# Optimization experiments

Hardware: AMD Instinct MI355X
Metric: run time of the kernel (lower is better)

## Reference

```python
import jax, jax.numpy as jnp
import numpy as np

B, V, VD = 4, 256, 3
H_DIM, N_HEADS = 512, 8
HEAD_DIM = H_DIM // N_HEADS
LN_EPS = 1e-5


def _ln(x, g, b):
    m = jnp.mean(x, axis=-1, keepdims=True)
    v = jnp.var(x, axis=-1, keepdims=True)
    return (x - m) * jax.lax.rsqrt(v + LN_EPS) * g + b


def setup_inputs() -> dict:
    key = jax.random.key(0)
    ks = jax.random.split(key, 20)
    s = lambda fan_in: 1.0 / np.sqrt(fan_in)
    return {
        "vertices": jax.random.normal(ks[0], (B, V, VD), jnp.float32),
        # vertex_proj: Linear(3 -> 512)
        "wp": jax.random.uniform(ks[1], (H_DIM, VD), jnp.float32, -s(VD), s(VD)),
        "bp": jax.random.uniform(ks[2], (H_DIM,), jnp.float32, -s(VD), s(VD)),
        # MultiheadAttention packed in-proj (3E, E) and out-proj (E, E)
        "in_w": jax.random.uniform(ks[3], (3 * H_DIM, H_DIM), jnp.float32, -s(H_DIM), s(H_DIM)),
        "in_b": jnp.zeros((3 * H_DIM,), jnp.float32),
        "out_w": jax.random.uniform(ks[4], (H_DIM, H_DIM), jnp.float32, -s(H_DIM), s(H_DIM)),
        "out_b": jnp.zeros((H_DIM,), jnp.float32),
        # edge_mlp: Linear(1024->512), LN(512), GELU, Linear(512->256), LN(256), GELU, Linear(256->1)
        "w1": jax.random.uniform(ks[5], (H_DIM, 2 * H_DIM), jnp.float32, -s(2 * H_DIM), s(2 * H_DIM)),
        "b1": jax.random.uniform(ks[6], (H_DIM,), jnp.float32, -s(2 * H_DIM), s(2 * H_DIM)),
        "g1": jnp.ones((H_DIM,), jnp.float32),
        "be1": jnp.zeros((H_DIM,), jnp.float32),
        "w2": jax.random.uniform(ks[7], (H_DIM // 2, H_DIM), jnp.float32, -s(H_DIM), s(H_DIM)),
        "b2": jax.random.uniform(ks[8], (H_DIM // 2,), jnp.float32, -s(H_DIM), s(H_DIM)),
        "g2": jnp.ones((H_DIM // 2,), jnp.float32),
        "be2": jnp.zeros((H_DIM // 2,), jnp.float32),
        "w3": jax.random.uniform(ks[9], (1, H_DIM // 2), jnp.float32, -s(H_DIM // 2), s(H_DIM // 2)),
        "b3": jax.random.uniform(ks[10], (1,), jnp.float32, -s(H_DIM // 2), s(H_DIM // 2)),
    }


def reference(vertices, wp, bp, in_w, in_b, out_w, out_b,
              w1, b1, g1, be1, w2, b2, g2, be2, w3, b3):
    # vertex projection: [B, V, H]
    x = jnp.einsum("bvd,hd->bvh", vertices, wp) + bp

    # self-attention (eval mode: dropout off)
    qkv = jnp.einsum("bvh,eh->bve", x, in_w) + in_b  # [B, V, 3H]
    q, k, v = jnp.split(qkv, 3, axis=-1)
    q = q.reshape(B, V, N_HEADS, HEAD_DIM)
    k = k.reshape(B, V, N_HEADS, HEAD_DIM)
    v = v.reshape(B, V, N_HEADS, HEAD_DIM)
    scores = jnp.einsum("bqnd,bknd->bnqk", q, k) / np.sqrt(HEAD_DIM)
    attn = jax.nn.softmax(scores, axis=-1)
    ctx = jnp.einsum("bnqk,bknd->bqnd", attn, v).reshape(B, V, H_DIM)
    attended = jnp.einsum("bvh,oh->bvo", ctx, out_w) + out_b
    x = x + attended  # residual

    # gather all upper-triangular vertex pairs: E = V*(V-1)/2
    ii, jj = jnp.triu_indices(V, k=1)
    v1 = x[:, ii, :]  # [B, E, H]
    v2 = x[:, jj, :]
    e = jnp.concatenate([v1, v2], axis=-1)  # [B, E, 2H]

    # edge MLP (exact-erf GELU like torch default)
    h = jnp.einsum("beh,oh->beo", e, w1) + b1
    h = jax.nn.gelu(_ln(h, g1, be1), approximate=False)
    h = jnp.einsum("beh,oh->beo", h, w2) + b2
    h = jax.nn.gelu(_ln(h, g2, be2), approximate=False)
    logits = jnp.einsum("beh,oh->beo", h, w3) + b3  # [B, E, 1]
    return jax.nn.sigmoid(logits[..., 0])  # [B, E]
```

## Files before the change

### kernel.cpp

```cpp
#include <hip/hip_runtime.h>
#include <hip/hip_bf16.h>
#include <hip/hip_fp16.h>

#define B_  4
#define V_  256
#define H_  512
#define E_  32640

typedef _Float16 half8 __attribute__((ext_vector_type(8)));
typedef float    f32x4 __attribute__((ext_vector_type(4)));

__device__ __forceinline__ float gelu_f(float x) {
    float u = x * 0.70710678118654752f;
    float a = fabsf(u);
    float t = __builtin_amdgcn_rcpf(fmaf(0.3275911f, a, 1.0f));
    float poly = t * fmaf(t, fmaf(t, fmaf(t, fmaf(t, 1.061405429f, -1.453152027f),
                                          1.421413741f), -0.284496736f), 0.254829592f);
    float ex = __expf(-u * u);
    float erfa = fmaf(-poly, ex, 1.0f);
    float erfu = copysignf(erfa, u);
    return 0.5f * x * (1.0f + erfu);
}

__device__ __forceinline__ float wred_add(float v) {
    #pragma unroll
    for (int off = 32; off > 0; off >>= 1) v += __shfl_xor(v, off, 64);
    return v;
}

__device__ __forceinline__ void split16(float v, _Float16* hi, _Float16* lo) {
    _Float16 h = (_Float16)v;
    *hi = h; *lo = (_Float16)(v - (float)h);
}

__device__ __forceinline__ size_t fmoff(int R, int row, int k) {
    return ((size_t)(k >> 3) * R + row) * 8 + (k & 7);
}

__global__ void k_setup(const float* __restrict__ verts, const float* __restrict__ wp,
                        const float* __restrict__ bp, float* __restrict__ x,
                        _Float16* __restrict__ xfh, _Float16* __restrict__ xfl,
                        const float* __restrict__ w2, _Float16* __restrict__ w2f,
                        int2* __restrict__ etab,
                        const float* __restrict__ in_w, _Float16* __restrict__ iwfh, _Float16* __restrict__ iwfl,
                        const float* __restrict__ out_w, _Float16* __restrict__ owfh, _Float16* __restrict__ owfl,
                        const float* __restrict__ w1, _Float16* __restrict__ w1fh, _Float16* __restrict__ w1fl) {
    int t = blockIdx.x * 256 + threadIdx.x;
    if (t < 524288) {
        int row = t >> 9, k = t & 511;
        const float* vr = verts + row * 3;
        const float* wr = wp + k * 3;
        float val = vr[0] * wr[0] + vr[1] * wr[1] + vr[2] * wr[2] + bp[k];
        x[t] = val;
        size_t fo = fmoff(1024, row, k);
        split16(val, xfh + fo, xfl + fo);
        return;
    }
    t -= 524288;
    if (t < 131072) {
        int col = t >> 9, k = t & 511;
        w2f[fmoff(256, col, k)] = (_Float16)w2[t];
        return;
    }
    t -= 131072;
    if (t < 32640) {
        double disc = (double)(2 * V_ - 1) * (2 * V_ - 1) - 8.0 * (double)t;
        int i = (int)((2 * V_ - 1 - sqrt(disc)) * 0.5);
        if (i < 0) i = 0;
        if (i > V_ - 2) i = V_ - 2;
        while (i < V_ - 2 && (i + 1) * (2 * V_ - 1 - (i + 1)) / 2 <= t) ++i;
        while (i > 0 && i * (2 * V_ - 1 - i) / 2 > t) --i;
        int j = t - i * (2 * V_ - 1 - i) / 2 + i + 1;
        etab[t] = make_int2(i, j);
        return;
    }
    t -= 32640;
    if (t < 786432) {
        int col = t >> 9, k = t & 511;
        size_t fo = fmoff(1536, col, k);
        split16(in_w[t], iwfh + fo, iwfl + fo);
        return;
    }
    t -= 786432;
    if (t < 262144) {
        int col = t >> 9, k = t & 511;
        size_t fo = fmoff(512, col, k);
        split16(out_w[t], owfh + fo, owfl + fo);
        return;
    }
    t -= 262144;
    if (t < 524288) {
        int col = t >> 9, k = t & 511;
        float v = (col < 512) ? w1[col * 1024 + k] : w1[(col - 512) * 1024 + 512 + k];
        size_t fo = fmoff(1024, col, k);
        split16(v, w1fh + fo, w1fl + fo);
    }
}

template<int MODE>
__global__ __launch_bounds__(256) void k_gemm_sp(
        const _Float16* __restrict__ Ahf, const _Float16* __restrict__ Alf,
        const _Float16* __restrict__ Whf, const _Float16* __restrict__ Wlf,
        const float* __restrict__ bias, const float* __restrict__ res,
        float* __restrict__ C, _Float16* __restrict__ Fh, _Float16* __restrict__ Fl,
        float* __restrict__ C2, _Float16* __restrict__ F2h, int N)
{
    const int tid = threadIdx.x;
    const int w = tid >> 6, l = tid & 63;
    const int lr = l & 15, lg = l >> 4;
    const int mg = w >> 1, ng = w & 1;
    const int row0 = blockIdx.y * 64 + mg * 32;
    const int col0 = blockIdx.x * 64 + ng * 32;

    f32x4 acc[2][2] = {};
    for (int kk = 0; kk < 16; ++kk) {
        const int kg = kk * 4 + lg;
        half8 ah[2], al[2], bh[2], bl[2];
        #pragma unroll
        for (int mi = 0; mi < 2; ++mi) {
            size_t off = ((size_t)kg * 1024 + row0 + mi * 16 + lr) * 8;
            ah[mi] = *(const half8*)(Ahf + off);
            al[mi] = *(const half8*)(Alf + off);
        }
        #pragma unroll
        for (int ni = 0; ni < 2; ++ni) {
            size_t off = ((size_t)kg * N + col0 + ni * 16 + lr) * 8;
            bh[ni] = *(const half8*)(Whf + off);
            bl[ni] = *(const half8*)(Wlf + off);
        }
        #pragma unroll
        for (int mi = 0; mi < 2; ++mi)
            #pragma unroll
            for (int ni = 0; ni < 2; ++ni) {
                acc[mi][ni] = __builtin_amdgcn_mfma_f32_16x16x32_f16(ah[mi], bh[ni], acc[mi][ni], 0, 0, 0);
                acc[mi][ni] = __builtin_amdgcn_mfma_f32_16x16x32_f16(ah[mi], bl[ni], acc[mi][ni], 0, 0, 0);
                acc[mi][ni] = __builtin_amdgcn_mfma_f32_16x16x32_f16(al[mi], bh[ni], acc[mi][ni], 0, 0, 0);
            }
    }
    #pragma unroll
    for (int mi = 0; mi < 2; ++mi)
        #pragma unroll
        for (int ni = 0; ni < 2; ++ni)
            #pragma unroll
            for (int r = 0; r < 4; ++r) {
                int row = row0 + mi * 16 + lg * 4 + r;
                int col = col0 + ni * 16 + lr;
                float v = acc[mi][ni][r];
                if (MODE == 1) {
                    size_t idx = (size_t)row * 512 + col;
                    v += bias[col] + res[idx];
                    C[idx] = v;
                    size_t fo = fmoff(1024, row, col);
                    split16(v, Fh + fo, Fl + fo);
                } else if (MODE == 2) {
                    if (col < 512) {
                        size_t idx = (size_t)row * 512 + col;
                        v += bias[col];
                        C[idx] = v;
                        Fh[fmoff(1024, row, col)] = (_Float16)v;
                    } else {
                        int c2 = col - 512;
                        C2[(size_t)row * 512 + c2] = v;
                        F2h[fmoff(1024, row, c2)] = (_Float16)v;
                    }
                } else {
                    v += bias[col];
                    int bb = row >> 8, tok = row & 255;
                    _Float16 hi = (_Float16)v;
                    _Float16 lo = (_Float16)(v - (float)hi);
                    if (col < 1024) {
                        int hp = col >> 6, d = col & 63;
                        size_t off = (((size_t)(bb * 16 + hp) * 8 + (d >> 3)) * 256 + tok) * 8 + (d & 7);
                        Fh[off] = hi; Fl[off] = lo;
                    } else {
                        int c = col - 1024, hp = c >> 6, d = c & 63;
                        size_t off = (((size_t)(bb * 8 + hp) * 32 + (tok >> 3)) * 64 + d) * 8 + (tok & 7);
                        ((_Float16*)C2)[off] = hi; F2h[off] = lo;
                    }
                }
            }
}

__global__ __launch_bounds__(256) void k_attn(
        const _Float16* __restrict__ QKh, const _Float16* __restrict__ QKl,
        const _Float16* __restrict__ Vh, const _Float16* __restrict__ Vl,
        _Float16* __restrict__ cfh, _Float16* __restrict__ cfl)
{
    extern __shared__ unsigned char smem[];
    const int tid = threadIdx.x;
    const int w = tid >> 6, l = tid & 63;
    const int lr = l & 15, lg = l >> 4;
    const int bh = blockIdx.x >> 2;
    const int b = bh >> 3, h = bh & 7;
    const int qb = blockIdx.x & 3;
    const int q0 = qb * 64 + w * 16;
    unsigned char* ph_base = smem + w * 16384;
    unsigned char* pl_base = ph_base + 8192;

    const size_t qbase = (size_t)(b * 16 + h) * 8;
    const size_t kbase = (size_t)(b * 16 + 8 + h) * 8;
    const size_t vbase = (size_t)(b * 8 + h) * 32;

    half8 qh[2], ql[2];
    #pragma unroll
    for (int ks = 0; ks < 2; ++ks) {
        size_t off = ((qbase + ks * 4 + lg) * 256 + q0 + lr) * 8;
        qh[ks] = *(const half8*)(QKh + off);
        ql[ks] = *(const half8*)(QKl + off);
    }

    f32x4 sc[16];
    #pragma unroll
    for (int kt = 0; kt < 16; ++kt) {
        f32x4 a = {};
        #pragma unroll
        for (int ks = 0; ks < 2; ++ks) {
            size_t off = ((kbase + ks * 4 + lg) * 256 + kt * 16 + lr) * 8;
            half8 kh = *(const half8*)(QKh + off);
            half8 kl = *(const half8*)(QKl + off);
            a = __builtin_amdgcn_mfma_f32_16x16x32_f16(qh[ks], kh, a, 0, 0, 0);
            a = __builtin_amdgcn_mfma_f32_16x16x32_f16(qh[ks], kl, a, 0, 0, 0);
            a = __builtin_amdgcn_mfma_f32_16x16x32_f16(ql[ks], kh, a, 0, 0, 0);
        }
        sc[kt] = a;
    }

    float mr[4] = {-1e30f, -1e30f, -1e30f, -1e30f};
    #pragma unroll
    for (int kt = 0; kt < 16; ++kt)
        #pragma unroll
        for (int r = 0; r < 4; ++r) mr[r] = fmaxf(mr[r], sc[kt][r]);
    #pragma unroll
    for (int off = 1; off < 16; off <<= 1)
        #pragma unroll
        for (int r = 0; r < 4; ++r) mr[r] = fmaxf(mr[r], __shfl_xor(mr[r], off, 64));

    float Ls[4] = {};
    #pragma unroll
    for (int kt = 0; kt < 16; ++kt)
        #pragma unroll
        for (int r = 0; r < 4; ++r) {
            float p = __expf((sc[kt][r] - mr[r]) * 0.125f);
            Ls[r] += p;
            _Float16 hp = (_Float16)p;
            _Float16 lp = (_Float16)(p - (float)hp);
            const int row = lg * 4 + r;
            unsigned off = row * 512 + (((unsigned)(kt * 16 + lr) * 2) ^ ((row & 7) << 4));
            *(_Float16*)(ph_base + off) = hp;
            *(_Float16*)(pl_base + off) = lp;
        }
    #pragma unroll
    for (int off = 1; off < 16; off <<= 1)
        #pragma unroll
        for (int r = 0; r < 4; ++r) Ls[r] += __shfl_xor(Ls[r], off, 64);

    __syncthreads();

    f32x4 o[4] = {};
    #pragma unroll
    for (int ks = 0; ks < 8; ++ks) {
        unsigned roff = lr * 512 + (((unsigned)(ks * 64 + lg * 16)) ^ ((lr & 7) << 4));
        half8 pah = *(const half8*)(ph_base + roff);
        half8 pal = *(const half8*)(pl_base + roff);
        #pragma unroll
        for (int nt = 0; nt < 4; ++nt) {
            size_t off = ((vbase + ks * 4 + lg) * 64 + nt * 16 + lr) * 8;
            half8 vbh = *(const half8*)(Vh + off);
            half8 vbl = *(const half8*)(Vl + off);
            o[nt] = __builtin_amdgcn_mfma_f32_16x16x32_f16(pah, vbh, o[nt], 0, 0, 0);
            o[nt] = __builtin_amdgcn_mfma_f32_16x16x32_f16(pah, vbl, o[nt], 0, 0, 0);
            o[nt] = __builtin_amdgcn_mfma_f32_16x16x32_f16(pal, vbh, o[nt], 0, 0, 0);
        }
    }

    float Linv[4];
    #pragma unroll
    for (int r = 0; r < 4; ++r) Linv[r] = 1.0f / Ls[r];
    #pragma unroll
    for (int nt = 0; nt < 4; ++nt)
        #pragma unroll
        for (int r = 0; r < 4; ++r) {
            float val = o[nt][r] * Linv[r];
            int row = b * 256 + q0 + lg * 4 + r;
            int col = h * 64 + nt * 16 + lr;
            size_t fo = fmoff(1024, row, col);
            split16(val, cfh + fo, cfl + fo);
        }
}

__global__ __launch_bounds__(256) void k_pair_stats(
        const _Float16* __restrict__ Ahf, const _Float16* __restrict__ Bhf,
        const float* __restrict__ Amat, const float* __restrict__ Bmat,
        float* __restrict__ P, float2* __restrict__ statsA, float2* __restrict__ statsB) {
    const int bid = blockIdx.x;
    const int tid = threadIdx.x;
    if (bid < 256) {
        const int t = bid * 4 + (tid >> 6);
        const int b = t >> 8, tt = t & 255;
        const int i0 = (tt >> 4) * 16, j0 = (tt & 15) * 16;
        const int l = tid & 63, lr = l & 15, lg = l >> 4;
        f32x4 acc = {};
        for (int kk = 0; kk < 16; ++kk) {
            const int kg = kk * 4 + lg;
            half8 af = *(const half8*)(Ahf + ((size_t)kg * 1024 + b * 256 + i0 + lr) * 8);
            half8 bf = *(const half8*)(Bhf + ((size_t)kg * 1024 + b * 256 + j0 + lr) * 8);
            acc = __builtin_amdgcn_mfma_f32_16x16x32_f16(af, bf, acc, 0, 0, 0);
        }
        #pragma unroll
        for (int r = 0; r < 4; ++r)
            P[((size_t)b << 16) + (size_t)(i0 + lg * 4 + r) * 256 + j0 + lr] = acc[r];
    } else {
        const int sid = bid - 256;
        const int slice = tid >> 4, lane = tid & 15;
        const int m = sid * 16 + slice;
        const float* src = (m < 1024 ? Amat + (size_t)m * 512 : Bmat + (size_t)(m - 1024) * 512);
        float s = 0.0f, sq = 0.0f;
        #pragma unroll
        for (int i = 0; i < 8; ++i) {
            f32x4 v = *(const f32x4*)(src + i * 64 + lane * 4);
            s  += v[0] + v[1] + v[2] + v[3];
            sq += v[0]*v[0] + v[1]*v[1] + v[2]*v[2] + v[3]*v[3];
        }
        #pragma unroll
        for (int off = 8; off > 0; off >>= 1) {
            s  += __shfl_xor(s, off, 64);
            sq += __shfl_xor(sq, off, 64);
        }
        if (lane == 0) {
            if (m < 1024) statsA[m] = make_float2(s, sq);
            else          statsB[m - 1024] = make_float2(s, sq);
        }
    }
}

__global__ __launch_bounds__(512, 4) void k_edge(
        const float* __restrict__ Am, const float* __restrict__ Bm,
        const _Float16* __restrict__ w2f,
        const float* __restrict__ g1, const float* __restrict__ be1,
        const float* __restrict__ b2, const float* __restrict__ g2,
        const float* __restrict__ be2, const float* __restrict__ w3,
        const float* __restrict__ b3, const int2* __restrict__ etab,
        const float2* __restrict__ statsA, const float2* __restrict__ statsB,
        const float* __restrict__ P, float* __restrict__ out)
{
    extern __shared__ unsigned char smem[];
    const int tid = threadIdx.x;
    const int w = tid >> 6;
    const int l = tid & 63;
    const int bid0 = blockIdx.x;
    const int swz = (bid0 & 7) * 255 + (bid0 >> 3);
    const int b  = swz / 510;
    const int eb = swz % 510;

    {
        const int el = l >> 3;
        const int kq = l & 7;
        const int e  = w * 8 + el;
        int2 ij = etab[eb * 64 + e];
        float2 sa = statsA[b * 256 + ij.x];
        float2 sb = statsB[b * 256 + ij.y];
        float pij = P[((size_t)b << 16) + ((size_t)ij.x << 8) + ij.y];
        float mean = (sa.x + sb.x) * (1.0f / 512.0f);
        float ex2  = (sa.y + sb.y + 2.0f * pij) * (1.0f / 512.0f);
        float rstd = rsqrtf(ex2 - mean * mean + 1e-5f);
        const float* ar = Am + (((size_t)(b * 256 + ij.x)) << 9);
        const float* br = Bm + (((size_t)(b * 256 + ij.y)) << 9);
        #pragma unroll
        for (int t = 0; t < 8; ++t) {
            const int kg = kq + 8 * t;
            const int k0 = kg * 8;
            f32x4 a0 = *(const f32x4*)(ar + k0);
            f32x4 a1 = *(const f32x4*)(ar + k0 + 4);
            f32x4 c0 = *(const f32x4*)(br + k0);
            f32x4 c1 = *(const f32x4*)(br + k0 + 4);
            f32x4 ga = *(const f32x4*)(g1 + k0);
            f32x4 gb = *(const f32x4*)(g1 + k0 + 4);
            f32x4 ea = *(const f32x4*)(be1 + k0);
            f32x4 ebv= *(const f32x4*)(be1 + k0 + 4);
            half8 hv;
            #pragma unroll
            for (int c = 0; c < 4; ++c) {
                float xa = ((a0[c] + c0[c]) - mean) * rstd * ga[c] + ea[c];
                float xb = ((a1[c] + c1[c]) - mean) * rstd * gb[c] + ebv[c];
                hv[c]     = (_Float16)gelu_f(xa);
                hv[c + 4] = (_Float16)gelu_f(xb);
            }
            *(half8*)(smem + kg * 1024 + ((e ^ (kg & 7)) << 4)) = hv;
        }
    }
    __syncthreads();

    f32x4 acc[4][2] = {};
    const int lg = l >> 4, lr = l & 15;
    const int col0 = w * 32;
    #pragma unroll
    for (int kk = 0; kk < 16; ++kk) {
        const int kg = kk * 4 + lg;
        half8 bf[2];
        #pragma unroll
        for (int ni = 0; ni < 2; ++ni)
            bf[ni] = *(const half8*)(w2f + ((size_t)kg * 256 + col0 + ni * 16 + lr) * 8);
        half8 af[4];
        #pragma unroll
        for (int mi = 0; mi < 4; ++mi)
            af[mi] = *(const half8*)(smem + kg * 1024 + (((mi * 16 + lr) ^ (kg & 7)) << 4));
        #pragma unroll
        for (int mi = 0; mi < 4; ++mi)
            #pragma unroll
            for (int ni = 0; ni < 2; ++ni)
                acc[mi][ni] = __builtin_amdgcn_mfma_f32_16x16x32_f16(af[mi], bf[ni], acc[mi][ni], 0, 0, 0);
    }
    __syncthreads();

    #pragma unroll
    for (int ni = 0; ni < 2; ++ni) {
        const int col = col0 + ni * 16 + lr;
        const float bb = b2[col];
        #pragma unroll
        for (int mi = 0; mi < 4; ++mi)
            #pragma unroll
            for (int r = 0; r < 4; ++r) {
                const int e = mi * 16 + lg * 4 + r;
                *(float*)(smem + e * 1024 + col * 4) = acc[mi][ni][r] + bb;
            }
    }
    __syncthreads();

    {
        const int o0 = l * 4;
        f32x4 g2v = *(const f32x4*)(g2 + o0);
        f32x4 e2v = *(const f32x4*)(be2 + o0);
        f32x4 w3v = *(const f32x4*)(w3 + o0);
        float b3s = b3[0];
        #pragma unroll
        for (int el = 0; el < 8; ++el) {
            const int e = w * 8 + el;
            f32x4 h = *(const f32x4*)(smem + e * 1024 + o0 * 4);
            float s  = h[0] + h[1] + h[2] + h[3];
            float sq = h[0]*h[0] + h[1]*h[1] + h[2]*h[2] + h[3]*h[3];
            s = wred_add(s); sq = wred_add(sq);
            float mean = s * (1.0f / 256.0f);
            float rstd = rsqrtf(sq * (1.0f / 256.0f) - mean * mean + 1e-5f);
            float part = 0.0f;
            #pragma unroll
            for (int c = 0; c < 4; ++c) {
                float xx = (h[c] - mean) * rstd * g2v[c] + e2v[c];
                part += gelu_f(xx) * w3v[c];
            }
            part = wred_add(part);
            if (l == 0)
                out[(size_t)b * E_ + eb * 64 + e] = 1.0f / (1.0f + __expf(-(part + b3s)));
        }
    }
}

extern "C" void kernel_launch(void* const* d_in, const int* in_sizes, int n_in,
                              void* d_out, int out_size, void* d_ws, size_t ws_size,
                              hipStream_t stream) {
    const float* verts = (const float*)d_in[0];
    const float* wp    = (const float*)d_in[1];
    const float* bp    = (const float*)d_in[2];
    const float* in_w  = (const float*)d_in[3];
    const float* in_b  = (const float*)d_in[4];
    const float* out_w = (const float*)d_in[5];
    const float* out_b = (const float*)d_in[6];
    const float* w1    = (const float*)d_in[7];
    const float* b1    = (const float*)d_in[8];
    const float* g1    = (const float*)d_in[9];
    const float* be1   = (const float*)d_in[10];
    const float* w2    = (const float*)d_in[11];
    const float* b2    = (const float*)d_in[12];
    const float* g2    = (const float*)d_in[13];
    const float* be2   = (const float*)d_in[14];
    const float* w3    = (const float*)d_in[15];
    const float* b3    = (const float*)d_in[16];
    float* out = (float*)d_out;

    const size_t MB = 1 << 20;
    char* W = (char*)d_ws;
    float*    x     = (float*)(W + 0);
    _Float16* xfh   = (_Float16*)(W + 2*MB);
    _Float16* xfl   = (_Float16*)(W + 3*MB);
    _Float16* QKfh  = (_Float16*)(W + 4*MB);
    _Float16* QKfl  = (_Float16*)(W + 6*MB);
    _Float16* Vfh   = (_Float16*)(W + 8*MB);
    _Float16* Vfl   = (_Float16*)(W + 9*MB);
    float*    Amat  = (float*)(W + 4*MB);
    float*    Bmat  = (float*)(W + 6*MB);
    _Float16* Ahf   = (_Float16*)(W + 8*MB);
    _Float16* Bhf   = (_Float16*)(W + 9*MB);
    _Float16* ctxfh = (_Float16*)(W + 10*MB);
    _Float16* ctxfl = (_Float16*)(W + 11*MB);
    _Float16* w2f   = (_Float16*)(W + 12*MB);
    int2*     etab  = (int2*)(W + 12*MB + 256*1024);
    float2*   statsA= (float2*)(W + 12*MB + 512*1024);
    float2*   statsB= (float2*)(W + 12*MB + 520*1024);
    _Float16* iwfh  = (_Float16*)(W + 13*MB);
    _Float16* iwfl  = (_Float16*)(W + 13*MB + 1536*1024);
    _Float16* owfh  = (_Float16*)(W + 16*MB);
    _Float16* owfl  = (_Float16*)(W + 16*MB + 512*1024);
    _Float16* w1fh  = (_Float16*)(W + 17*MB);
    _Float16* w1fl  = (_Float16*)(W + 18*MB);
    float*    P     = (float*)(W + 19*MB);

    k_setup<<<dim3(8832), dim3(256), 0, stream>>>(verts, wp, bp, x, xfh, xfl,
                                                  w2, w2f, etab, in_w, iwfh, iwfl,
                                                  out_w, owfh, owfl, w1, w1fh, w1fl);
    k_gemm_sp<3><<<dim3(24, 16), dim3(256), 0, stream>>>(xfh, xfl, iwfh, iwfl, in_b, nullptr,
                                                         nullptr, QKfh, QKfl, (float*)Vfh, Vfl, 1536);
    k_attn<<<dim3(128), dim3(256), 65536, stream>>>(QKfh, QKfl, Vfh, Vfl, ctxfh, ctxfl);
    k_gemm_sp<1><<<dim3(8, 16), dim3(256), 0, stream>>>(ctxfh, ctxfl, owfh, owfl, out_b, x,
                                                        x, xfh, xfl, nullptr, nullptr, 512);
    k_gemm_sp<2><<<dim3(16, 16), dim3(256), 0, stream>>>(xfh, xfl, w1fh, w1fl, b1, nullptr,
                                                         Amat, Ahf, nullptr, Bmat, Bhf, 1024);
    k_pair_stats<<<dim3(384), dim3(256), 0, stream>>>(Ahf, Bhf, Amat, Bmat, P, statsA, statsB);
    k_edge<<<dim3(B_ * 510), dim3(512), 65536, stream>>>(Amat, Bmat, w2f,
                                                         g1, be1, b2, g2, be2, w3, b3,
                                                         etab, statsA, statsB, P, out);
}
```

Measured before the change: 265.7 us.

## Halve edge-kernel tile and interleave fp16 hi/lo pairs for attention buffers

The edge MLP kernel now handles 32 edges per block instead of 64. That halves its shared memory to 32KB, doubles the grid, and raises the launch-bounds occupancy hint from 4 to 8. The goal is more resident blocks to hide latency, at the cost of reading the w2 weights twice as often overall. Separately, the QKV, V and context split-fp16 buffers now store hi and lo interleaved as one 32-bit word. This replaces paired 16-bit stores and separate loads with single packed accesses plus some bit unpacking in the attention and out-projection GEMM.

```diff
diff --git a/kernel.cpp b/kernel.cpp
--- a/kernel.cpp
+++ b/kernel.cpp
@@ -9,6 +9,7 @@
 
 typedef _Float16 half8 __attribute__((ext_vector_type(8)));
 typedef float    f32x4 __attribute__((ext_vector_type(4)));
+typedef unsigned int uint4v __attribute__((ext_vector_type(4)));
 
 __device__ __forceinline__ float gelu_f(float x) {
     float u = x * 0.70710678118654752f;
@@ -31,6 +32,26 @@
 __device__ __forceinline__ void split16(float v, _Float16* hi, _Float16* lo) {
     _Float16 h = (_Float16)v;
     *hi = h; *lo = (_Float16)(v - (float)h);
+}
+
+__device__ __forceinline__ unsigned packf(float v) {
+    _Float16 h = (_Float16)v;
+    _Float16 l = (_Float16)(v - (float)h);
+    unsigned hu = (unsigned)__builtin_bit_cast(unsigned short, h);
+    unsigned lu = (unsigned)__builtin_bit_cast(unsigned short, l);
+    return hu | (lu << 16);
+}
+
+__device__ __forceinline__ void unpk8(const unsigned* p, half8& hi, half8& lo) {
+    uint4v a = *(const uint4v*)p;
+    uint4v b = *(const uint4v*)(p + 4);
+    uint4v hw, lw;
+    hw[0] = (a[0] & 0xFFFFu) | (a[1] << 16);  lw[0] = (a[0] >> 16) | (a[1] & 0xFFFF0000u);
+    hw[1] = (a[2] & 0xFFFFu) | (a[3] << 16);  lw[1] = (a[2] >> 16) | (a[3] & 0xFFFF0000u);
+    hw[2] = (b[0] & 0xFFFFu) | (b[1] << 16);  lw[2] = (b[0] >> 16) | (b[1] & 0xFFFF0000u);
+    hw[3] = (b[2] & 0xFFFFu) | (b[3] << 16);  lw[3] = (b[2] >> 16) | (b[3] & 0xFFFF0000u);
+    hi = __builtin_bit_cast(half8, hw);
+    lo = __builtin_bit_cast(half8, lw);
 }
 
 __device__ __forceinline__ size_t fmoff(int R, int row, int k) {
@@ -119,8 +140,12 @@
         #pragma unroll
         for (int mi = 0; mi < 2; ++mi) {
             size_t off = ((size_t)kg * 1024 + row0 + mi * 16 + lr) * 8;
-            ah[mi] = *(const half8*)(Ahf + off);
-            al[mi] = *(const half8*)(Alf + off);
+            if (MODE == 1) {
+                unpk8((const unsigned*)Ahf + off, ah[mi], al[mi]);
+            } else {
+                ah[mi] = *(const half8*)(Ahf + off);
+                al[mi] = *(const half8*)(Alf + off);
+            }
         }
         #pragma unroll
         for (int ni = 0; ni < 2; ++ni) {
@@ -166,25 +191,22 @@
                 } else {
                     v += bias[col];
                     int bb = row >> 8, tok = row & 255;
-                    _Float16 hi = (_Float16)v;
-                    _Float16 lo = (_Float16)(v - (float)hi);
                     if (col < 1024) {
                         int hp = col >> 6, d = col & 63;
                         size_t off = (((size_t)(bb * 16 + hp) * 8 + (d >> 3)) * 256 + tok) * 8 + (d & 7);
-                        Fh[off] = hi; Fl[off] = lo;
+                        ((unsigned*)Fh)[off] = packf(v);
                     } else {
                         int c = col - 1024, hp = c >> 6, d = c & 63;
                         size_t off = (((size_t)(bb * 8 + hp) * 32 + (tok >> 3)) * 64 + d) * 8 + (tok & 7);
-                        ((_Float16*)C2)[off] = hi; F2h[off] = lo;
+                        ((unsigned*)C2)[off] = packf(v);
                     }
                 }
             }
 }
 
 __global__ __launch_bounds__(256) void k_attn(
-        const _Float16* __restrict__ QKh, const _Float16* __restrict__ QKl,
-        const _Float16* __restrict__ Vh, const _Float16* __restrict__ Vl,
-        _Float16* __restrict__ cfh, _Float16* __restrict__ cfl)
+        const unsigned* __restrict__ QKp, const unsigned* __restrict__ Vp,
+        unsigned* __restrict__ ctxp)
 {
     extern __shared__ unsigned char smem[];
     const int tid = threadIdx.x;
@@ -205,8 +227,7 @@
     #pragma unroll
     for (int ks = 0; ks < 2; ++ks) {
         size_t off = ((qbase + ks * 4 + lg) * 256 + q0 + lr) * 8;
-        qh[ks] = *(const half8*)(QKh + off);
-        ql[ks] = *(const half8*)(QKl + off);
+        unpk8(QKp + off, qh[ks], ql[ks]);
     }
 
     f32x4 sc[16];
@@ -216,8 +237,8 @@
         #pragma unroll
         for (int ks = 0; ks < 2; ++ks) {
             size_t off = ((kbase + ks * 4 + lg) * 256 + kt * 16 + lr) * 8;
-            half8 kh = *(const half8*)(QKh + off);
-            half8 kl = *(const half8*)(QKl + off);
+            half8 kh, kl;
+            unpk8(QKp + off, kh, kl);
             a = __builtin_amdgcn_mfma_f32_16x16x32_f16(qh[ks], kh, a, 0, 0, 0);
             a = __builtin_amdgcn_mfma_f32_16x16x32_f16(qh[ks], kl, a, 0, 0, 0);
             a = __builtin_amdgcn_mfma_f32_16x16x32_f16(ql[ks], kh, a, 0, 0, 0);
@@ -265,8 +286,8 @@
         #pragma unroll
         for (int nt = 0; nt < 4; ++nt) {
             size_t off = ((vbase + ks * 4 + lg) * 64 + nt * 16 + lr) * 8;
-            half8 vbh = *(const half8*)(Vh + off);
-            half8 vbl = *(const half8*)(Vl + off);
+            half8 vbh, vbl;
+            unpk8(Vp + off, vbh, vbl);
             o[nt] = __builtin_amdgcn_mfma_f32_16x16x32_f16(pah, vbh, o[nt], 0, 0, 0);
             o[nt] = __builtin_amdgcn_mfma_f32_16x16x32_f16(pah, vbl, o[nt], 0, 0, 0);
             o[nt] = __builtin_amdgcn_mfma_f32_16x16x32_f16(pal, vbh, o[nt], 0, 0, 0);
@@ -283,8 +304,7 @@
             float val = o[nt][r] * Linv[r];
             int row = b * 256 + q0 + lg * 4 + r;
             int col = h * 64 + nt * 16 + lr;
-            size_t fo = fmoff(1024, row, col);
-            split16(val, cfh + fo, cfl + fo);
+            ctxp[fmoff(1024, row, col)] = packf(val);
         }
 }
 
@@ -333,7 +353,7 @@
     }
 }
 
-__global__ __launch_bounds__(512, 4) void k_edge(
+__global__ __launch_bounds__(512, 8) void k_edge(
         const float* __restrict__ Am, const float* __restrict__ Bm,
         const _Float16* __restrict__ w2f,
         const float* __restrict__ g1, const float* __restrict__ be1,
@@ -348,15 +368,14 @@
     const int w = tid >> 6;
     const int l = tid & 63;
     const int bid0 = blockIdx.x;
-    const int swz = (bid0 & 7) * 255 + (bid0 >> 3);
-    const int b  = swz / 510;
-    const int eb = swz % 510;
+    const int swz = (bid0 & 7) * 510 + (bid0 >> 3);
+    const int b  = swz / 1020;
+    const int eb = swz % 1020;
 
     {
-        const int el = l >> 3;
-        const int kq = l & 7;
-        const int e  = w * 8 + el;
-        int2 ij = etab[eb * 64 + e];
+        const int e  = w * 4 + (l >> 4);
+        const int kq = l & 15;
+        int2 ij = etab[eb * 32 + e];
         float2 sa = statsA[b * 256 + ij.x];
         float2 sb = statsB[b * 256 + ij.y];
         float pij = P[((size_t)b << 16) + ((size_t)ij.x << 8) + ij.y];
@@ -366,8 +385,8 @@
         const float* ar = Am + (((size_t)(b * 256 + ij.x)) << 9);
         const float* br = Bm + (((size_t)(b * 256 + ij.y)) << 9);
         #pragma unroll
-        for (int t = 0; t < 8; ++t) {
-            const int kg = kq + 8 * t;
+        for (int t = 0; t < 4; ++t) {
+            const int kg = kq + 16 * t;
             const int k0 = kg * 8;
             f32x4 a0 = *(const f32x4*)(ar + k0);
             f32x4 a1 = *(const f32x4*)(ar + k0 + 4);
@@ -385,12 +404,12 @@
                 hv[c]     = (_Float16)gelu_f(xa);
                 hv[c + 4] = (_Float16)gelu_f(xb);
             }
-            *(half8*)(smem + kg * 1024 + ((e ^ (kg & 7)) << 4)) = hv;
+            *(half8*)(smem + kg * 512 + ((e ^ (kg & 7)) << 4)) = hv;
         }
     }
     __syncthreads();
 
-    f32x4 acc[4][2] = {};
+    f32x4 acc[2][2] = {};
     const int lg = l >> 4, lr = l & 15;
     const int col0 = w * 32;
     #pragma unroll
@@ -400,12 +419,12 @@
         #pragma unroll
         for (int ni = 0; ni < 2; ++ni)
             bf[ni] = *(const half8*)(w2f + ((size_t)kg * 256 + col0 + ni * 16 + lr) * 8);
-        half8 af[4];
-        #pragma unroll
-        for (int mi = 0; mi < 4; ++mi)
-            af[mi] = *(const half8*)(smem + kg * 1024 + (((mi * 16 + lr) ^ (kg & 7)) << 4));
-        #pragma unroll
-        for (int mi = 0; mi < 4; ++mi)
+        half8 af[2];
+        #pragma unroll
+        for (int mi = 0; mi < 2; ++mi)
+            af[mi] = *(const half8*)(smem + kg * 512 + (((mi * 16 + lr) ^ (kg & 7)) << 4));
+        #pragma unroll
+        for (int mi = 0; mi < 2; ++mi)
             #pragma unroll
             for (int ni = 0; ni < 2; ++ni)
                 acc[mi][ni] = __builtin_amdgcn_mfma_f32_16x16x32_f16(af[mi], bf[ni], acc[mi][ni], 0, 0, 0);
@@ -417,7 +436,7 @@
         const int col = col0 + ni * 16 + lr;
         const float bb = b2[col];
         #pragma unroll
-        for (int mi = 0; mi < 4; ++mi)
+        for (int mi = 0; mi < 2; ++mi)
             #pragma unroll
             for (int r = 0; r < 4; ++r) {
                 const int e = mi * 16 + lg * 4 + r;
@@ -433,8 +452,8 @@
         f32x4 w3v = *(const f32x4*)(w3 + o0);
         float b3s = b3[0];
         #pragma unroll
-        for (int el = 0; el < 8; ++el) {
-            const int e = w * 8 + el;
+        for (int el = 0; el < 4; ++el) {
+            const int e = w * 4 + el;
             f32x4 h = *(const f32x4*)(smem + e * 1024 + o0 * 4);
             float s  = h[0] + h[1] + h[2] + h[3];
             float sq = h[0]*h[0] + h[1]*h[1] + h[2]*h[2] + h[3]*h[3];
@@ -449,7 +468,7 @@
             }
             part = wred_add(part);
             if (l == 0)
-                out[(size_t)b * E_ + eb * 64 + e] = 1.0f / (1.0f + __expf(-(part + b3s)));
+                out[(size_t)b * E_ + eb * 32 + e] = 1.0f / (1.0f + __expf(-(part + b3s)));
         }
     }
 }
@@ -481,16 +500,13 @@
     float*    x     = (float*)(W + 0);
     _Float16* xfh   = (_Float16*)(W + 2*MB);
     _Float16* xfl   = (_Float16*)(W + 3*MB);
-    _Float16* QKfh  = (_Float16*)(W + 4*MB);
-    _Float16* QKfl  = (_Float16*)(W + 6*MB);
-    _Float16* Vfh   = (_Float16*)(W + 8*MB);
-    _Float16* Vfl   = (_Float16*)(W + 9*MB);
+    unsigned* QKp   = (unsigned*)(W + 4*MB);
+    unsigned* Vp    = (unsigned*)(W + 8*MB);
     float*    Amat  = (float*)(W + 4*MB);
     float*    Bmat  = (float*)(W + 6*MB);
     _Float16* Ahf   = (_Float16*)(W + 8*MB);
     _Float16* Bhf   = (_Float16*)(W + 9*MB);
-    _Float16* ctxfh = (_Float16*)(W + 10*MB);
-    _Float16* ctxfl = (_Float16*)(W + 11*MB);
+    unsigned* ctxp  = (unsigned*)(W + 10*MB);
     _Float16* w2f   = (_Float16*)(W + 12*MB);
     int2*     etab  = (int2*)(W + 12*MB + 256*1024);
     float2*   statsA= (float2*)(W + 12*MB + 512*1024);
@@ -507,14 +523,16 @@
                                                   w2, w2f, etab, in_w, iwfh, iwfl,
                                                   out_w, owfh, owfl, w1, w1fh, w1fl);
     k_gemm_sp<3><<<dim3(24, 16), dim3(256), 0, stream>>>(xfh, xfl, iwfh, iwfl, in_b, nullptr,
-                                                         nullptr, QKfh, QKfl, (float*)Vfh, Vfl, 1536);
-    k_attn<<<dim3(128), dim3(256), 65536, stream>>>(QKfh, QKfl, Vfh, Vfl, ctxfh, ctxfl);
-    k_gemm_sp<1><<<dim3(8, 16), dim3(256), 0, stream>>>(ctxfh, ctxfl, owfh, owfl, out_b, x,
+                                                         nullptr, (_Float16*)QKp, nullptr,
+                                                         (float*)Vp, nullptr, 1536);
+    k_attn<<<dim3(128), dim3(256), 65536, stream>>>(QKp, Vp, ctxp);
+    k_gemm_sp<1><<<dim3(8, 16), dim3(256), 0, stream>>>((const _Float16*)ctxp, nullptr,
+                                                        owfh, owfl, out_b, x,
                                                         x, xfh, xfl, nullptr, nullptr, 512);
     k_gemm_sp<2><<<dim3(16, 16), dim3(256), 0, stream>>>(xfh, xfl, w1fh, w1fl, b1, nullptr,
                                                          Amat, Ahf, nullptr, Bmat, Bhf, 1024);
     k_pair_stats<<<dim3(384), dim3(256), 0, stream>>>(Ahf, Bhf, Amat, Bmat, P, statsA, statsB);
-    k_edge<<<dim3(B_ * 510), dim3(512), 65536, stream>>>(Amat, Bmat, w2f,
-                                                         g1, be1, b2, g2, be2, w3, b3,
-                                                         etab, statsA, statsB, P, out);
-}
+    k_edge<<<dim3(B_ * 1020), dim3(512), 32768, stream>>>(Amat, Bmat, w2f,
+                                                          g1, be1, b2, g2, be2, w3, b3,
+                                                          etab, statsA, statsB, P, out);
+}
```

Result: slower. 278.6 us (+4.9%).
